# Kernel optimization log

Hardware: AMD Instinct MI355X
Metric: run time of the kernel (lower is better)

## Reference

```python
import jax, jax.numpy as jnp
import numpy as np

EMBED = 1024
HIDDEN = 4 * EMBED
NUM_EXPERTS = 8
TOP_K = 2


def setup_inputs() -> dict:
    key = jax.random.key(0)
    k_in, k_w1, k_b1, k_w2, k_b2 = jax.random.split(key, 5)
    s1 = 1.0 / np.sqrt(EMBED)
    s2 = 1.0 / np.sqrt(HIDDEN)
    return {
        "inputs": jax.random.normal(k_in, (8, 4096, EMBED), dtype=jnp.float32),
        "w1": jax.random.uniform(k_w1, (EMBED, HIDDEN), jnp.float32, -s1, s1),
        "b1": jax.random.uniform(k_b1, (HIDDEN,), jnp.float32, -s1, s1),
        "w2": jax.random.uniform(k_w2, (HIDDEN, NUM_EXPERTS), jnp.float32, -s2, s2),
        "b2": jax.random.uniform(k_b2, (NUM_EXPERTS,), jnp.float32, -s2, s2),
    }


def reference(inputs, w1, b1, w2, b2):
    # MLP scorer: [B,S,E] -> [B,S,H] -> [B,S,num_experts]
    h = jax.nn.relu(jnp.einsum("bse,eh->bsh", inputs, w1) + b1)
    score = jnp.einsum("bsh,hn->bsn", h, w2) + b2
    # top-k over expert dim
    _, topk_idx = jax.lax.top_k(score, TOP_K)  # [B,S,K]
    # scatter mask: True at top-k positions
    mask = jax.nn.one_hot(topk_idx, NUM_EXPERTS, dtype=jnp.bool_).any(axis=-2)  # [B,S,N]
    masked = jnp.where(mask, score, -jnp.inf)
    router_output = jax.nn.softmax(masked, axis=-1)
    return router_output, topk_idx
```

## Files before the change

kernel.cpp:

```cpp
#include <hip/hip_runtime.h>

#define T_TOK 32768
#define EDIM  1024
#define HDIM  4096
#define NEXP  8
#define TAU   1.0e-3f
#define MAXR  8192


typedef _Float16 f16x8 __attribute__((ext_vector_type(8)));
typedef _Float16 f16x4 __attribute__((ext_vector_type(4)));
typedef __attribute__((ext_vector_type(4))) float f32x4;
#define MFMA16(a, b, c) __builtin_amdgcn_mfma_f32_16x16x32_f16(a, b, c, 0, 0, 0)

__device__ __forceinline__ void gload16(const void* g, void* l) {
    __builtin_amdgcn_global_load_lds(
        (const __attribute__((address_space(1))) void*)g,
        (__attribute__((address_space(3))) void*)l, 16, 0, 0);
}

__global__ __launch_bounds__(256) void split_x_kernel(
    const float* __restrict__ x, _Float16* __restrict__ hi, int n4)
{
    int i = blockIdx.x * 256 + threadIdx.x;
    int stride = gridDim.x * 256;
    for (; i < n4; i += stride) {
        float4 v = ((const float4*)x)[i];
        f16x4 h;
        h[0] = (_Float16)v.x; h[1] = (_Float16)v.y;
        h[2] = (_Float16)v.z; h[3] = (_Float16)v.w;
        *(f16x4*)&hi[i * 4] = h;
    }
}

__global__ __launch_bounds__(256) void split_w1t_kernel(
    const float* __restrict__ w1, _Float16* __restrict__ thi)
{
    __shared__ float t[64][65];
    const int ht = blockIdx.x;
    const int et = blockIdx.y;
    const int tid = threadIdx.x;
    const int er = tid >> 6, hc = tid & 63;
#pragma unroll
    for (int rr = 0; rr < 16; ++rr) {
        int e = rr * 4 + er;
        t[e][hc] = w1[(size_t)(et * 64 + e) * HDIM + ht * 64 + hc];
    }
    __syncthreads();
    const int hl = tid >> 2, eg = tid & 3;
    size_t base = (size_t)(ht * 64 + hl) * EDIM + et * 64 + eg * 16;
#pragma unroll
    for (int q = 0; q < 4; ++q) {
        f16x4 a;
#pragma unroll
        for (int z = 0; z < 4; ++z) a[z] = (_Float16)t[eg * 16 + q * 4 + z][hl];
        *(f16x4*)&thi[base + q * 4] = a;
    }
}

__global__ __launch_bounds__(256, 2) void mfma_score_kernel(
    const _Float16* __restrict__ xhi, const _Float16* __restrict__ whi,
    const float* __restrict__ b1, const float* __restrict__ w2,
    float* __restrict__ part)
{
    __shared__ __align__(16) _Float16 A3[3 * 8192];
    __shared__ __align__(16) _Float16 B3[3 * 4096];

    const int bid = blockIdx.x;
    const int lg  = (bid & 7) * 512 + (bid >> 3);
    const int ht  = (lg >> 9) * 4 + (lg & 3);
    const int mt  = (lg & 511) >> 2;
    const int m0 = mt * 256;
    const int h0 = ht * 128;
    const int tid = threadIdx.x;
    const int l = tid & 63;
    const int wid = tid >> 6;
    const int wm = wid >> 1, wn = wid & 1;

    const int srow = tid >> 2;
    const int sg = (tid & 3) ^ ((srow >> 1) & 3);
    const int ldst = tid * 16;

    const int lrow = l & 15, lslot = l >> 4;
    const int rslot = lslot ^ ((lrow >> 1) & 3);
    const int aoff = (wm * 128 + lrow) * 64 + rslot * 16;
    const int boff = (wn * 64 + lrow) * 64 + rslot * 16;

    f32x4 acc[8][4];
    const f32x4 zz = {0.f, 0.f, 0.f, 0.f};
#pragma unroll
    for (int i = 0; i < 8; ++i)
#pragma unroll
        for (int j = 0; j < 4; ++j) acc[i][j] = zz;

    auto stage = [&](int s, int bb) {
        const int k0 = s * 32;
        char* Ab = (char*)A3 + bb * 16384;
        char* Bb = (char*)B3 + bb * 8192;
#pragma unroll
        for (int r = 0; r < 4; ++r)
            gload16(xhi + (size_t)(m0 + r * 64 + srow) * EDIM + sg * 8 + k0,
                    Ab + r * 4096 + ldst);
#pragma unroll
        for (int r = 0; r < 2; ++r)
            gload16(whi + (size_t)(h0 + r * 64 + srow) * EDIM + sg * 8 + k0,
                    Bb + r * 4096 + ldst);
    };
    auto compute = [&](int bb) {
        const char* Ab = (const char*)A3 + bb * 16384;
        const char* Bb = (const char*)B3 + bb * 8192;
        f16x8 ah[8];
#pragma unroll
        for (int mf = 0; mf < 8; ++mf)
            ah[mf] = *(const f16x8*)(Ab + aoff + mf * 1024);
        __builtin_amdgcn_s_setprio(1);
#pragma unroll
        for (int nf = 0; nf < 4; ++nf) {
            f16x8 bh = *(const f16x8*)(Bb + boff + nf * 1024);
#pragma unroll
            for (int mf = 0; mf < 8; ++mf)
                acc[mf][nf] = MFMA16(ah[mf], bh, acc[mf][nf]);
        }
        __builtin_amdgcn_s_setprio(0);
    };

#define WAITV6 do { asm volatile("s_waitcnt vmcnt(6)" ::: "memory"); \
                    __builtin_amdgcn_sched_barrier(0); } while (0)
#define WAITV0 do { asm volatile("s_waitcnt vmcnt(0)" ::: "memory"); \
                    __builtin_amdgcn_sched_barrier(0); } while (0)
#define BARR   do { __builtin_amdgcn_s_barrier(); \
                    __builtin_amdgcn_sched_barrier(0); } while (0)

    stage(0, 0);
    stage(1, 1);

    for (int t = 0; t < 30; t += 3) {
        WAITV6; BARR; stage(t + 2, (t + 2) % 3); compute(0);
        WAITV6; BARR; stage(t + 3, (t + 3) % 3); compute(1);
        WAITV6; BARR; stage(t + 4, (t + 4) % 3); compute(2);
    }
    WAITV6; BARR; compute(0);
    WAITV0; BARR; compute(1);

#undef WAITV6
#undef WAITV0
#undef BARR

    float b1r[4], w2r[4][8];
#pragma unroll
    for (int nf = 0; nf < 4; ++nf) {
        int h = h0 + wn * 64 + nf * 16 + lrow;
        b1r[nf] = b1[h];
#pragma unroll
        for (int n = 0; n < 8; ++n) w2r[nf][n] = w2[(size_t)h * NEXP + n];
    }

    const int b0 = l & 1, b1b = (l >> 1) & 1, b2 = (l >> 2) & 1, b3 = (l >> 3) & 1;
    const int regf = (b0 << 1) | b1b;
    const int n0e  = b2 * 4 + b3 * 2;
    float outq[8][2];

#pragma unroll
    for (int q = 0; q < 8; ++q) {
        float v[32];
#pragma unroll
        for (int i = 0; i < 32; ++i) v[i] = 0.f;
#pragma unroll
        for (int reg = 0; reg < 4; ++reg)
#pragma unroll
            for (int nf = 0; nf < 4; ++nf) {
                float hv = fmaxf(acc[q][nf][reg] + b1r[nf], 0.f);
#pragma unroll
                for (int n = 0; n < 8; ++n)
                    v[reg * 8 + n] = fmaf(hv, w2r[nf][n], v[reg * 8 + n]);
            }
        float t1[16];
#pragma unroll
        for (int i = 0; i < 16; ++i) {
            float keep = b0 ? v[i + 16] : v[i];
            float send = b0 ? v[i] : v[i + 16];
            t1[i] = keep + __shfl_xor(send, 1);
        }
        float t2[8];
#pragma unroll
        for (int i = 0; i < 8; ++i) {
            float keep = b1b ? t1[i + 8] : t1[i];
            float send = b1b ? t1[i] : t1[i + 8];
            t2[i] = keep + __shfl_xor(send, 2);
        }
        float t3[4];
#pragma unroll
        for (int i = 0; i < 4; ++i) {
            float keep = b2 ? t2[i + 4] : t2[i];
            float send = b2 ? t2[i] : t2[i + 4];
            t3[i] = keep + __shfl_xor(send, 4);
        }
#pragma unroll
        for (int j = 0; j < 2; ++j) {
            float keep = b3 ? t3[j + 2] : t3[j];
            float send = b3 ? t3[j] : t3[j + 2];
            outq[q][j] = keep + __shfl_xor(send, 8);
        }
    }

    __syncthreads();
    float* red = (float*)A3;
    if (wn == 1) {
#pragma unroll
        for (int q = 0; q < 8; ++q) {
            red[(wm * 64 + l) * 16 + q * 2 + 0] = outq[q][0];
            red[(wm * 64 + l) * 16 + q * 2 + 1] = outq[q][1];
        }
    }
    __syncthreads();
    if (wn == 0) {
#pragma unroll
        for (int q = 0; q < 8; ++q) {
            float a = outq[q][0] + red[(wm * 64 + l) * 16 + q * 2 + 0];
            float b = outq[q][1] + red[(wm * 64 + l) * 16 + q * 2 + 1];
            int rl = wm * 128 + q * 16 + lslot * 4 + regf;
            *(float2*)&part[((size_t)ht * T_TOK + m0 + rl) * NEXP + n0e] =
                make_float2(a, b);
        }
    }
}

__global__ void zero_counter_kernel(int* c) {
    if (threadIdx.x == 0 && blockIdx.x == 0) *c = 0;
}

__global__ __launch_bounds__(256) void router_finish_kernel(
    const float* __restrict__ part, const float* __restrict__ b2,
    float* __restrict__ out, int nparts, int* __restrict__ counter,
    int* __restrict__ list)
{
    int t = blockIdx.x * 256 + threadIdx.x;
    if (t >= T_TOK) return;

    float s[NEXP];
#pragma unroll
    for (int n = 0; n < NEXP; ++n) s[n] = 0.f;
    for (int p = 0; p < nparts; ++p) {
        const float* ps = part + (size_t)p * T_TOK * NEXP + (size_t)t * NEXP;
        float4 v0 = *reinterpret_cast<const float4*>(ps);
        float4 v1 = *reinterpret_cast<const float4*>(ps + 4);
        s[0] += v0.x; s[1] += v0.y; s[2] += v0.z; s[3] += v0.w;
        s[4] += v1.x; s[5] += v1.y; s[6] += v1.z; s[7] += v1.w;
    }
#pragma unroll
    for (int n = 0; n < NEXP; ++n) s[n] += b2[n];

    int i1 = 0; float v1 = s[0];
#pragma unroll
    for (int n = 1; n < NEXP; ++n) { if (s[n] > v1) { v1 = s[n]; i1 = n; } }
    int i2 = -1; float v2 = -3.402823466e38f;
#pragma unroll
    for (int n = 0; n < NEXP; ++n) { if (n != i1 && s[n] > v2) { v2 = s[n]; i2 = n; } }
    float v3 = -3.402823466e38f;
#pragma unroll
    for (int n = 0; n < NEXP; ++n) { if (n != i1 && n != i2 && s[n] > v3) v3 = s[n]; }

    if ((v1 - v2) < TAU || (v2 - v3) < TAU) {
        int pos = atomicAdd(counter, 1);
        list[pos] = t;
    }

    float e2 = expf(v2 - v1);
    float denom = 1.f + e2;
    float p1 = 1.f / denom;
    float p2 = e2 / denom;
#pragma unroll
    for (int n = 0; n < NEXP; ++n)
        out[(size_t)t * NEXP + n] = (n == i1) ? p1 : ((n == i2) ? p2 : 0.f);
    out[(size_t)T_TOK * NEXP + (size_t)t * 2 + 0] = (float)i1;
    out[(size_t)T_TOK * NEXP + (size_t)t * 2 + 1] = (float)i2;
}

__global__ __launch_bounds__(256) void gather_x_kernel(
    const float* __restrict__ x, const int* __restrict__ counter,
    const int* __restrict__ list, float* __restrict__ xg)
{
    int cnt = *counter; if (cnt > MAXR) cnt = MAXR;
    for (int g = blockIdx.x; g < cnt; g += gridDim.x) {
        const int t = list[g];
        float4 v = ((const float4*)(x + (size_t)t * EDIM))[threadIdx.x];
        ((float4*)(xg + (size_t)g * EDIM))[threadIdx.x] = v;
    }
}

__global__ __launch_bounds__(256) void refine_gemm_kernel(
    const float* __restrict__ xg, const float* __restrict__ w1,
    const float* __restrict__ b1, const float* __restrict__ w2,
    const int* __restrict__ counter, float* __restrict__ rpart)
{
    int cnt = *counter; if (cnt > MAXR) cnt = MAXR;
    const int m0 = blockIdx.y * 64;
    if (m0 >= cnt) return;
    const int ht = blockIdx.x;
    const int h0 = ht * 128;
    const int tid = threadIdx.x;
    const int tx = tid & 15, ty = tid >> 4;

    __shared__ float xs[16][68];
    __shared__ float wsh[16][128];

    float acc[4][8];
#pragma unroll
    for (int i = 0; i < 4; ++i)
#pragma unroll
        for (int j = 0; j < 8; ++j) acc[i][j] = 0.f;

    const int lk = tid & 15, lt = tid >> 4;
    const int lh = tid & 127, lkg = tid >> 7;

    for (int k0 = 0; k0 < EDIM; k0 += 16) {
        __syncthreads();
#pragma unroll
        for (int r = 0; r < 4; ++r)
            xs[lk][lt + r * 16] = xg[(size_t)(m0 + lt + r * 16) * EDIM + k0 + lk];
#pragma unroll
        for (int r = 0; r < 8; ++r)
            wsh[lkg + r * 2][lh] = w1[(size_t)(k0 + lkg + r * 2) * HDIM + h0 + lh];
        __syncthreads();
#pragma unroll
        for (int k = 0; k < 16; ++k) {
            float a[4], b[8];
#pragma unroll
            for (int i = 0; i < 4; ++i) a[i] = xs[k][ty * 4 + i];
            *reinterpret_cast<float4*>(&b[0]) = *reinterpret_cast<const float4*>(&wsh[k][tx * 8]);
            *reinterpret_cast<float4*>(&b[4]) = *reinterpret_cast<const float4*>(&wsh[k][tx * 8 + 4]);
#pragma unroll
            for (int i = 0; i < 4; ++i)
#pragma unroll
                for (int j = 0; j < 8; ++j)
                    acc[i][j] = fmaf(a[i], b[j], acc[i][j]);
        }
    }

    float sred[4][NEXP];
#pragma unroll
    for (int i = 0; i < 4; ++i) {
        float hv[8];
#pragma unroll
        for (int j = 0; j < 8; ++j)
            hv[j] = fmaxf(acc[i][j] + b1[h0 + tx * 8 + j], 0.f);
#pragma unroll
        for (int n = 0; n < NEXP; ++n) {
            float ssum = 0.f;
#pragma unroll
            for (int j = 0; j < 8; ++j)
                ssum = fmaf(hv[j], w2[(size_t)(h0 + tx * 8 + j) * NEXP + n], ssum);
            sred[i][n] = ssum;
        }
    }
#pragma unroll
    for (int i = 0; i < 4; ++i)
#pragma unroll
        for (int n = 0; n < NEXP; ++n) {
            float v = sred[i][n];
            v += __shfl_xor(v, 1);
            v += __shfl_xor(v, 2);
            v += __shfl_xor(v, 4);
            v += __shfl_xor(v, 8);
            sred[i][n] = v;
        }

    if (tx == 0) {
#pragma unroll
        for (int i = 0; i < 4; ++i) {
            int g = m0 + ty * 4 + i;
            if (g < cnt) {
#pragma unroll
                for (int n = 0; n < NEXP; ++n)
                    rpart[((size_t)g * 32 + ht) * NEXP + n] = sred[i][n];
            }
        }
    }
}

__global__ __launch_bounds__(256) void refine_final_kernel(
    const int* __restrict__ counter, const int* __restrict__ list,
    const float* __restrict__ rpart, const float* __restrict__ b2,
    float* __restrict__ out)
{
    int cnt = *counter; if (cnt > MAXR) cnt = MAXR;
    const int g = blockIdx.x * 256 + threadIdx.x;
    if (g >= cnt) return;
    const int t = list[g];
    float s[NEXP];
#pragma unroll
    for (int n = 0; n < NEXP; ++n) s[n] = b2[n];
    for (int r = 0; r < 32; ++r)
#pragma unroll
        for (int n = 0; n < NEXP; ++n)
            s[n] += rpart[((size_t)g * 32 + r) * NEXP + n];

    int i1 = 0; float v1 = s[0];
#pragma unroll
    for (int n = 1; n < NEXP; ++n) { if (s[n] > v1) { v1 = s[n]; i1 = n; } }
    int i2 = -1; float v2 = -3.402823466e38f;
#pragma unroll
    for (int n = 0; n < NEXP; ++n) { if (n != i1 && s[n] > v2) { v2 = s[n]; i2 = n; } }

    float e2 = expf(v2 - v1);
    float denom = 1.f + e2;
    float p1 = 1.f / denom;
    float p2 = e2 / denom;
#pragma unroll
    for (int n = 0; n < NEXP; ++n)
        out[(size_t)t * NEXP + n] = (n == i1) ? p1 : ((n == i2) ? p2 : 0.f);
    out[(size_t)T_TOK * NEXP + (size_t)t * 2 + 0] = (float)i1;
    out[(size_t)T_TOK * NEXP + (size_t)t * 2 + 1] = (float)i2;
}

#define BM 128
#define BH 128
#define BK 16
#define NHT (HDIM / BH)

__global__ __launch_bounds__(256) void score_gemm_kernel(
    const float* __restrict__ x, const float* __restrict__ w1,
    const float* __restrict__ b1, const float* __restrict__ w2,
    float* __restrict__ dst)
{
    __shared__ float xs[BK][BM + 4];
    __shared__ float wsh[BK][BH];
    __shared__ float w2s[BH * NEXP];
    __shared__ float b1s[BH];

    const int htile = blockIdx.x;
    const int mtile = blockIdx.y;
    const int h0 = htile * BH;
    const int m0 = mtile * BM;
    const int tid = threadIdx.x;
    const int tx = tid & 15;
    const int ty = tid >> 4;

    {
        float4 v = *reinterpret_cast<const float4*>(&w2[(size_t)h0 * NEXP + tid * 4]);
        *reinterpret_cast<float4*>(&w2s[tid * 4]) = v;
        if (tid < BH) b1s[tid] = b1[h0 + tid];
    }

    float acc[8][8];
#pragma unroll
    for (int i = 0; i < 8; ++i)
#pragma unroll
        for (int j = 0; j < 8; ++j) acc[i][j] = 0.f;

    const int e_off = tid & 15;
    const int t_row = tid >> 4;
    const int h_off = tid & 127;
    const int k_off = tid >> 7;

    for (int k0 = 0; k0 < EDIM; k0 += BK) {
        __syncthreads();
#pragma unroll
        for (int r = 0; r < 8; ++r) {
            int tok = t_row + r * 16;
            xs[e_off][tok] = x[(size_t)(m0 + tok) * EDIM + k0 + e_off];
        }
#pragma unroll
        for (int r = 0; r < 8; ++r) {
            int k = k_off + r * 2;
            wsh[k][h_off] = w1[(size_t)(k0 + k) * HDIM + h0 + h_off];
        }
        __syncthreads();
#pragma unroll
        for (int k = 0; k < BK; ++k) {
            float a[8], b[8];
            *reinterpret_cast<float4*>(&a[0]) = *reinterpret_cast<const float4*>(&xs[k][ty * 8]);
            *reinterpret_cast<float4*>(&a[4]) = *reinterpret_cast<const float4*>(&xs[k][ty * 8 + 4]);
            *reinterpret_cast<float4*>(&b[0]) = *reinterpret_cast<const float4*>(&wsh[k][tx * 8]);
            *reinterpret_cast<float4*>(&b[4]) = *reinterpret_cast<const float4*>(&wsh[k][tx * 8 + 4]);
#pragma unroll
            for (int i = 0; i < 8; ++i)
#pragma unroll
                for (int j = 0; j < 8; ++j)
                    acc[i][j] = fmaf(a[i], b[j], acc[i][j]);
        }
    }

    float sred[8][NEXP];
#pragma unroll
    for (int i = 0; i < 8; ++i) {
        float hv[8];
#pragma unroll
        for (int j = 0; j < 8; ++j)
            hv[j] = fmaxf(acc[i][j] + b1s[tx * 8 + j], 0.f);
#pragma unroll
        for (int n = 0; n < NEXP; ++n) {
            float ssum = 0.f;
#pragma unroll
            for (int j = 0; j < 8; ++j)
                ssum = fmaf(hv[j], w2s[(tx * 8 + j) * NEXP + n], ssum);
            sred[i][n] = ssum;
        }
    }
#pragma unroll
    for (int i = 0; i < 8; ++i)
#pragma unroll
        for (int n = 0; n < NEXP; ++n) {
            float v = sred[i][n];
            v += __shfl_xor(v, 1);
            v += __shfl_xor(v, 2);
            v += __shfl_xor(v, 4);
            v += __shfl_xor(v, 8);
            sred[i][n] = v;
        }

    if (tx == 0) {
        float* slice = dst + (size_t)htile * T_TOK * NEXP;
#pragma unroll
        for (int i = 0; i < 8; ++i)
#pragma unroll
            for (int n = 0; n < NEXP; ++n)
                slice[(size_t)(m0 + ty * 8 + i) * NEXP + n] = sred[i][n];
    }
}

__global__ __launch_bounds__(256) void finish_simple_kernel(
    const float* __restrict__ part, const float* __restrict__ b2,
    float* __restrict__ out, int nparts)
{
    int t = blockIdx.x * 256 + threadIdx.x;
    if (t >= T_TOK) return;
    float s[NEXP];
#pragma unroll
    for (int n = 0; n < NEXP; ++n) s[n] = 0.f;
    for (int p = 0; p < nparts; ++p) {
        const float* ps = part + (size_t)p * T_TOK * NEXP + (size_t)t * NEXP;
        float4 v0 = *reinterpret_cast<const float4*>(ps);
        float4 v1 = *reinterpret_cast<const float4*>(ps + 4);
        s[0] += v0.x; s[1] += v0.y; s[2] += v0.z; s[3] += v0.w;
        s[4] += v1.x; s[5] += v1.y; s[6] += v1.z; s[7] += v1.w;
    }
#pragma unroll
    for (int n = 0; n < NEXP; ++n) s[n] += b2[n];
    int i1 = 0; float v1 = s[0];
#pragma unroll
    for (int n = 1; n < NEXP; ++n) { if (s[n] > v1) { v1 = s[n]; i1 = n; } }
    int i2 = -1; float v2 = -3.402823466e38f;
#pragma unroll
    for (int n = 0; n < NEXP; ++n) { if (n != i1 && s[n] > v2) { v2 = s[n]; i2 = n; } }
    float e2 = expf(v2 - v1);
    float denom = 1.f + e2;
    float p1 = 1.f / denom;
    float p2 = e2 / denom;
#pragma unroll
    for (int n = 0; n < NEXP; ++n)
        out[(size_t)t * NEXP + n] = (n == i1) ? p1 : ((n == i2) ? p2 : 0.f);
    out[(size_t)T_TOK * NEXP + (size_t)t * 2 + 0] = (float)i1;
    out[(size_t)T_TOK * NEXP + (size_t)t * 2 + 1] = (float)i2;
}

extern "C" void kernel_launch(void* const* d_in, const int* in_sizes, int n_in,
                              void* d_out, int out_size, void* d_ws, size_t ws_size,
                              hipStream_t stream)
{
    const float* x  = (const float*)d_in[0];
    const float* w1 = (const float*)d_in[1];
    const float* b1 = (const float*)d_in[2];
    const float* w2 = (const float*)d_in[3];
    const float* b2 = (const float*)d_in[4];
    float* out = (float*)d_out;

    char* ws = (char*)d_ws;
    _Float16* xhi = (_Float16*)ws;
    _Float16* whi = (_Float16*)(ws + 67108864);
    float* part   = (float*)(ws + 75497472);
    int* counter  = (int*)(ws + 109051904);
    int* list     = (int*)(ws + 109052928);
    float* xg     = (float*)(ws + 109184000);
    float* rpart  = (float*)(ws + 142738432);
    const size_t NEED = 151127040;

    if (ws_size >= NEED) {
        split_x_kernel<<<2048, 256, 0, stream>>>(x, xhi, (T_TOK * EDIM) / 4);
        dim3 tg(64, 16);
        split_w1t_kernel<<<tg, 256, 0, stream>>>(w1, whi);
        mfma_score_kernel<<<4096, 256, 0, stream>>>(xhi, whi, b1, w2, part);
        zero_counter_kernel<<<1, 64, 0, stream>>>(counter);
        router_finish_kernel<<<T_TOK / 256, 256, 0, stream>>>(part, b2, out, 32,
                                                              counter, list);
        gather_x_kernel<<<256, 256, 0, stream>>>(x, counter, list, xg);
        dim3 rg(32, MAXR / 64);
        refine_gemm_kernel<<<rg, 256, 0, stream>>>(xg, w1, b1, w2, counter, rpart);
        refine_final_kernel<<<MAXR / 256, 256, 0, stream>>>(counter, list, rpart,
                                                            b2, out);
    } else {
        float* p1 = (float*)d_ws;
        dim3 grid(NHT, T_TOK / BM);
        score_gemm_kernel<<<grid, 256, 0, stream>>>(x, w1, b1, w2, p1);
        finish_simple_kernel<<<T_TOK / 256, 256, 0, stream>>>(p1, b2, out, NHT);
    }
}
```

Measured before the change: 700.0 us.

## Enlarge score GEMM tile to 256x256 with 8 waves and double buffering

The fp16 MFMA scoring GEMM now runs 512-thread blocks, each computing a 256x256 token-by-hidden tile instead of 256x128. The hidden partial sums per token drop from 32 to 16, so the partial buffer and the finish kernel's reduction shrink. The three-stage LDS pipeline becomes a two-stage double buffer with one barrier-synchronised loop, and fragment loads are split into two halves to hold fewer A registers at once. The aim is more data reuse per LDS load and less partial-sum traffic. In exchange there is less prefetch depth, more barriers per step, and a larger cross-wave epilogue reduction.

```diff
diff --git a/kernel.cpp b/kernel.cpp
--- a/kernel.cpp
+++ b/kernel.cpp
@@ -6,6 +6,7 @@
 #define NEXP  8
 #define TAU   1.0e-3f
 #define MAXR  8192
+#define NHT_F 16
 
 
 typedef _Float16 f16x8 __attribute__((ext_vector_type(8)));
@@ -58,33 +59,35 @@
     }
 }
 
-__global__ __launch_bounds__(256, 2) void mfma_score_kernel(
+__global__ __launch_bounds__(512, 2) void mfma_score_kernel(
     const _Float16* __restrict__ xhi, const _Float16* __restrict__ whi,
     const float* __restrict__ b1, const float* __restrict__ w2,
     float* __restrict__ part)
 {
-    __shared__ __align__(16) _Float16 A3[3 * 8192];
-    __shared__ __align__(16) _Float16 B3[3 * 4096];
+    __shared__ __align__(16) _Float16 Ax[2][256 * 32];
+    __shared__ __align__(16) _Float16 Bx[2][256 * 32];
 
     const int bid = blockIdx.x;
-    const int lg  = (bid & 7) * 512 + (bid >> 3);
-    const int ht  = (lg >> 9) * 4 + (lg & 3);
-    const int mt  = (lg & 511) >> 2;
+    const int lg  = (bid & 7) * 256 + (bid >> 3);
+    const int ht  = lg >> 7;
+    const int mt  = lg & 127;
     const int m0 = mt * 256;
-    const int h0 = ht * 128;
+    const int h0 = ht * 256;
     const int tid = threadIdx.x;
     const int l = tid & 63;
     const int wid = tid >> 6;
-    const int wm = wid >> 1, wn = wid & 1;
+    const int wm = wid >> 2, wn = wid & 3;
 
     const int srow = tid >> 2;
     const int sg = (tid & 3) ^ ((srow >> 1) & 3);
+    const _Float16* xsrc = xhi + (size_t)(m0 + srow) * EDIM + sg * 8;
+    const _Float16* wsrc = whi + (size_t)(h0 + srow) * EDIM + sg * 8;
     const int ldst = tid * 16;
 
     const int lrow = l & 15, lslot = l >> 4;
     const int rslot = lslot ^ ((lrow >> 1) & 3);
-    const int aoff = (wm * 128 + lrow) * 64 + rslot * 16;
-    const int boff = (wn * 64 + lrow) * 64 + rslot * 16;
+    const int abase = (wm * 128 + lrow) * 64 + rslot * 16;
+    const int bbase = (wn * 64 + lrow) * 64 + rslot * 16;
 
     f32x4 acc[8][4];
     const f32x4 zz = {0.f, 0.f, 0.f, 0.f};
@@ -93,58 +96,61 @@
 #pragma unroll
         for (int j = 0; j < 4; ++j) acc[i][j] = zz;
 
-    auto stage = [&](int s, int bb) {
-        const int k0 = s * 32;
-        char* Ab = (char*)A3 + bb * 16384;
-        char* Bb = (char*)B3 + bb * 8192;
-#pragma unroll
-        for (int r = 0; r < 4; ++r)
-            gload16(xhi + (size_t)(m0 + r * 64 + srow) * EDIM + sg * 8 + k0,
-                    Ab + r * 4096 + ldst);
-#pragma unroll
-        for (int r = 0; r < 2; ++r)
-            gload16(whi + (size_t)(h0 + r * 64 + srow) * EDIM + sg * 8 + k0,
-                    Bb + r * 4096 + ldst);
+    auto stage = [&](int t, int b) {
+        const int k0 = t * 32;
+        gload16(xsrc + k0,                      (char*)Ax[b] + ldst);
+        gload16(xsrc + (size_t)128 * EDIM + k0, (char*)Ax[b] + 8192 + ldst);
+        gload16(wsrc + k0,                      (char*)Bx[b] + ldst);
+        gload16(wsrc + (size_t)128 * EDIM + k0, (char*)Bx[b] + 8192 + ldst);
     };
-    auto compute = [&](int bb) {
-        const char* Ab = (const char*)A3 + bb * 16384;
-        const char* Bb = (const char*)B3 + bb * 8192;
-        f16x8 ah[8];
-#pragma unroll
-        for (int mf = 0; mf < 8; ++mf)
-            ah[mf] = *(const f16x8*)(Ab + aoff + mf * 1024);
+
+    stage(0, 0);
+
+    for (int t = 0; t < 32; ++t) {
+        const int b = t & 1;
+        if (t < 31) {
+            stage(t + 1, b ^ 1);
+            asm volatile("s_waitcnt vmcnt(4)" ::: "memory");
+        } else {
+            asm volatile("s_waitcnt vmcnt(0)" ::: "memory");
+        }
+        __builtin_amdgcn_sched_barrier(0);
+        __builtin_amdgcn_s_barrier();
+        __builtin_amdgcn_sched_barrier(0);
+
+        f16x8 bh[4], ah[4];
+#pragma unroll
+        for (int nf = 0; nf < 4; ++nf)
+            bh[nf] = *(const f16x8*)((const char*)Bx[b] + bbase + nf * 1024);
+#pragma unroll
+        for (int mf = 0; mf < 4; ++mf)
+            ah[mf] = *(const f16x8*)((const char*)Ax[b] + abase + mf * 1024);
+        asm volatile("s_waitcnt lgkmcnt(0)" ::: "memory");
+        __builtin_amdgcn_sched_barrier(0);
         __builtin_amdgcn_s_setprio(1);
 #pragma unroll
-        for (int nf = 0; nf < 4; ++nf) {
-            f16x8 bh = *(const f16x8*)(Bb + boff + nf * 1024);
-#pragma unroll
-            for (int mf = 0; mf < 8; ++mf)
-                acc[mf][nf] = MFMA16(ah[mf], bh, acc[mf][nf]);
-        }
+        for (int nf = 0; nf < 4; ++nf)
+#pragma unroll
+            for (int mf = 0; mf < 4; ++mf)
+                acc[mf][nf] = MFMA16(ah[mf], bh[nf], acc[mf][nf]);
         __builtin_amdgcn_s_setprio(0);
-    };
-
-#define WAITV6 do { asm volatile("s_waitcnt vmcnt(6)" ::: "memory"); \
-                    __builtin_amdgcn_sched_barrier(0); } while (0)
-#define WAITV0 do { asm volatile("s_waitcnt vmcnt(0)" ::: "memory"); \
-                    __builtin_amdgcn_sched_barrier(0); } while (0)
-#define BARR   do { __builtin_amdgcn_s_barrier(); \
-                    __builtin_amdgcn_sched_barrier(0); } while (0)
-
-    stage(0, 0);
-    stage(1, 1);
-
-    for (int t = 0; t < 30; t += 3) {
-        WAITV6; BARR; stage(t + 2, (t + 2) % 3); compute(0);
-        WAITV6; BARR; stage(t + 3, (t + 3) % 3); compute(1);
-        WAITV6; BARR; stage(t + 4, (t + 4) % 3); compute(2);
-    }
-    WAITV6; BARR; compute(0);
-    WAITV0; BARR; compute(1);
-
-#undef WAITV6
-#undef WAITV0
-#undef BARR
+
+#pragma unroll
+        for (int mf = 0; mf < 4; ++mf)
+            ah[mf] = *(const f16x8*)((const char*)Ax[b] + abase + (4 + mf) * 1024);
+        asm volatile("s_waitcnt lgkmcnt(0)" ::: "memory");
+        __builtin_amdgcn_sched_barrier(0);
+        __builtin_amdgcn_s_setprio(1);
+#pragma unroll
+        for (int nf = 0; nf < 4; ++nf)
+#pragma unroll
+            for (int mf = 0; mf < 4; ++mf)
+                acc[4 + mf][nf] = MFMA16(ah[mf], bh[nf], acc[4 + mf][nf]);
+        __builtin_amdgcn_s_setprio(0);
+
+        __builtin_amdgcn_s_barrier();
+        __builtin_amdgcn_sched_barrier(0);
+    }
 
     float b1r[4], w2r[4][8];
 #pragma unroll
@@ -204,23 +210,27 @@
     }
 
     __syncthreads();
-    float* red = (float*)A3;
-    if (wn == 1) {
+    float* red = (float*)Ax;
+    if (wn != 0) {
 #pragma unroll
         for (int q = 0; q < 8; ++q) {
-            red[(wm * 64 + l) * 16 + q * 2 + 0] = outq[q][0];
-            red[(wm * 64 + l) * 16 + q * 2 + 1] = outq[q][1];
+            red[((wn - 1) * 128 + wm * 64 + l) * 16 + q * 2 + 0] = outq[q][0];
+            red[((wn - 1) * 128 + wm * 64 + l) * 16 + q * 2 + 1] = outq[q][1];
         }
     }
     __syncthreads();
     if (wn == 0) {
 #pragma unroll
         for (int q = 0; q < 8; ++q) {
-            float a = outq[q][0] + red[(wm * 64 + l) * 16 + q * 2 + 0];
-            float b = outq[q][1] + red[(wm * 64 + l) * 16 + q * 2 + 1];
+            float a = outq[q][0], bb = outq[q][1];
+#pragma unroll
+            for (int w = 0; w < 3; ++w) {
+                a  += red[(w * 128 + wm * 64 + l) * 16 + q * 2 + 0];
+                bb += red[(w * 128 + wm * 64 + l) * 16 + q * 2 + 1];
+            }
             int rl = wm * 128 + q * 16 + lslot * 4 + regf;
             *(float2*)&part[((size_t)ht * T_TOK + m0 + rl) * NEXP + n0e] =
-                make_float2(a, b);
+                make_float2(a, bb);
         }
     }
 }
@@ -569,19 +579,19 @@
     _Float16* xhi = (_Float16*)ws;
     _Float16* whi = (_Float16*)(ws + 67108864);
     float* part   = (float*)(ws + 75497472);
-    int* counter  = (int*)(ws + 109051904);
-    int* list     = (int*)(ws + 109052928);
-    float* xg     = (float*)(ws + 109184000);
-    float* rpart  = (float*)(ws + 142738432);
-    const size_t NEED = 151127040;
+    int* counter  = (int*)(ws + 92274688);
+    int* list     = (int*)(ws + 92275712);
+    float* xg     = (float*)(ws + 92406784);
+    float* rpart  = (float*)(ws + 125961216);
+    const size_t NEED = 134349824;
 
     if (ws_size >= NEED) {
         split_x_kernel<<<2048, 256, 0, stream>>>(x, xhi, (T_TOK * EDIM) / 4);
         dim3 tg(64, 16);
         split_w1t_kernel<<<tg, 256, 0, stream>>>(w1, whi);
-        mfma_score_kernel<<<4096, 256, 0, stream>>>(xhi, whi, b1, w2, part);
+        mfma_score_kernel<<<2048, 512, 0, stream>>>(xhi, whi, b1, w2, part);
         zero_counter_kernel<<<1, 64, 0, stream>>>(counter);
-        router_finish_kernel<<<T_TOK / 256, 256, 0, stream>>>(part, b2, out, 32,
+        router_finish_kernel<<<T_TOK / 256, 256, 0, stream>>>(part, b2, out, NHT_F,
                                                               counter, list);
         gather_x_kernel<<<256, 256, 0, stream>>>(x, counter, list, xg);
         dim3 rg(32, MAXR / 64);
```

Measured after the change: 873.7 us. 24.8% more time.
